# Optimization experiments

Hardware: AMD Instinct MI355X
Metric: run time of the kernel (lower is better)

Reference implementation:

```python
import jax, jax.numpy as jnp
import numpy as np

L, M, DIN, DEM, DH, GH, DOUT = 4, 4, 128, 64, 400, 256, 8
B = 16384
EPS = 1e-5


def setup_inputs() -> dict:
    key = jax.random.key(0)
    ks = iter(jax.random.split(key, 48))
    def p(shape, s=0.05):
        return jax.random.normal(next(ks), shape, jnp.float32) * s
    return dict(
        x=p((B, DIN), 1.0), embedding_input=p((B, DEM), 1.0),
        base_w1=p((DIN, DH)), base_b1=p((DH,)), base_w2=p((DH, DH)), base_b2=p((DH,)),
        em_w=p((DEM, DH)), em_b=p((DH,)),
        gfc_w1=p((DH, GH)), gfc_b1=p((GH,)), gfc_w2=p((GH, GH)), gfc_b2=p((GH,)),
        gw0_w=p((GH, M * M)), gw0_b=p((M * M,)),
        cond1_w=p((M * M, GH)), cond1_b=p((GH,)), gw1_w=p((GH, M * M)), gw1_b=p((M * M,)),
        cond2_w=p((2 * M * M, GH)), cond2_b=p((GH,)), gw2_w=p((GH, M * M)), gw2_b=p((M * M,)),
        condL_w=p((3 * M * M, GH)), condL_b=p((GH,)), gwL_w=p((GH, M)), gwL_b=p((M,)),
        bn1_g=1.0 + p((L, M, DH)), bn1_b=p((L, M, DH)),
        mod_W=p((L, M, DH, DH)), mod_b=p((L, M, DH)),
        bn2_g=1.0 + p((L, M, DH)), bn2_b=p((L, M, DH)),
        last_w=p((DH, DOUT)), last_b=p((DOUT,)),
    )


def _bn(h, g, b):
    # training-mode BatchNorm1d over batch axis; h:[B,M,D], g,b:[M,D]
    mu = h.mean(axis=0)
    var = ((h - mu) ** 2).mean(axis=0)  # biased variance, as torch BN
    return (h - mu) / jnp.sqrt(var + EPS) * g + b


def reference(x, embedding_input,
              base_w1, base_b1, base_w2, base_b2, em_w, em_b,
              gfc_w1, gfc_b1, gfc_w2, gfc_b2,
              gw0_w, gw0_b, cond1_w, cond1_b, gw1_w, gw1_b,
              cond2_w, cond2_b, gw2_w, gw2_b,
              condL_w, condL_b, gwL_w, gwL_b,
              bn1_g, bn1_b, mod_W, mod_b, bn2_g, bn2_b,
              last_w, last_b):
    relu = jax.nn.relu
    b = x.shape[0]
    # base MLP (last activation = identity)
    out = relu(x @ base_w1 + base_b1) @ base_w2 + base_b2          # [B,DH]
    # embedding MLP (single layer, identity last activation)
    emb = embedding_input @ em_w + em_b                            # [B,DH]
    emb = emb * out                                                # cond_ob
    out = relu(out)
    # gating trunk
    emb = relu(emb)
    emb = relu(emb @ gfc_w1 + gfc_b1)
    emb = emb @ gfc_w2 + gfc_b2                                    # [B,GH]
    # routing weight 0
    raw0 = relu(emb) @ gw0_w + gw0_b                               # [B,M*M]
    w0 = jax.nn.softmax(raw0.reshape(b, M, M), axis=-1)
    weights = [w0]
    flat = [w0.reshape(b, M * M)]
    # cascaded routing weights (num_layers-2 = 2 extra)
    for cw, cb, gw, gb in ((cond1_w, cond1_b, gw1_w, gw1_b),
                           (cond2_w, cond2_b, gw2_w, gw2_b)):
        cond = jnp.concatenate(flat, axis=-1) @ cw + cb            # [B,GH]
        cond = relu(cond * emb)
        w = jax.nn.softmax((cond @ gw + gb).reshape(b, M, M), axis=-1)
        weights.append(w)
        flat.append(w.reshape(b, M * M))
    # last (per-module) gating weight
    cond = jnp.concatenate(flat, axis=-1) @ condL_w + condL_b
    cond = relu(cond * emb)
    last_weight = jax.nn.softmax(cond @ gwL_w + gwL_b, axis=-1)    # [B,M]
    # module layer 0: all modules see the same input
    h = jnp.broadcast_to(out[:, None, :], (b, M, DH))
    h = _bn(h, bn1_g[0], bn1_b[0])
    mo = jnp.einsum('bmi,mio->bmo', h, mod_W[0]) + mod_b[0]
    mo = _bn(mo, bn2_g[0], bn2_b[0])                               # [B,M,DH]
    # cascaded module layers with soft routing
    for i in range(1, L):
        mi = relu(jnp.einsum('bkd,bjk->bjd', mo, weights[i - 1]))  # dispatch/combine
        h = _bn(mi, bn1_g[i], bn1_b[i])
        mo = jnp.einsum('bmi,mio->bmo', h, mod_W[i]) + mod_b[i]
        mo = _bn(mo, bn2_g[i], bn2_b[i])
    out = relu(jnp.einsum('bmd,bm->bd', mo, last_weight))
    return out @ last_w + last_b
```

## Files before the change

kernel.cpp:

```cpp
#include <hip/hip_runtime.h>
#include <hip/hip_bf16.h>

typedef __bf16 bf16_t;
typedef __bf16 bf16x8 __attribute__((ext_vector_type(8)));
typedef __bf16 bf16x4 __attribute__((ext_vector_type(4)));
typedef float  f32x4  __attribute__((ext_vector_type(4)));

#define BN_   16384
#define DIN_  128
#define DEM_  64
#define DH_   400
#define DHP_  416
#define DHA_  512
#define GH_   256
#define MM_   4
#define EPS_  1e-5f
#define PCOLS 448
#define NCH   128
#define NCHMI 256

__global__ __launch_bounds__(256) void k_detect_probe(const unsigned* __restrict__ w,
                                                      int* __restrict__ flag,
                                                      int* __restrict__ layC)
{
  __shared__ int cnt[256];
  int c = 0;
  for (int i = 0; i < 16; ++i) {
    unsigned v = w[threadIdx.x * 16 + i];
    float lo = __uint_as_float((v & 0xffffu) << 16);
    if (!(fabsf(lo) < 1e4f)) ++c;
  }
  cnt[threadIdx.x] = c;
  __syncthreads();
  if (threadIdx.x == 0) {
    int t = 0;
    for (int i = 0; i < 256; ++i) t += cnt[i];
    flag[0] = (t > 64) ? 1 : 0;
  }
  if (threadIdx.x < 64) {
    int l = threadIdx.x;
    bf16x8 av, bv;
#pragma unroll
    for (int e = 0; e < 8; ++e) { av[e] = (bf16_t)0.f; bv[e] = (bf16_t)0.f; }
    if ((l >> 4) == 0) av[0] = (bf16_t)(float)(l & 15);
    if (l == 0)        bv[0] = (bf16_t)1.f;
    f32x4 acc = {0.f, 0.f, 0.f, 0.f};
    acc = __builtin_amdgcn_mfma_f32_16x16x32_bf16(av, bv, acc, 0, 0, 0);
    if (l == 1) layC[0] = (acc[0] > 0.5f) ? 1 : 0;
  }
}

#define NS_ 26
struct SmallTab {
  const void* src[NS_];
  bf16_t*     dst[NS_];
  int         n[NS_];
};

struct Cvt2 {
  const void* src1; bf16_t* dst1; int n1;
  const void* src2; bf16_t* dst2; int n2;
};

#define NT_ 9
#define CVZ 8
struct TransTab {
  const void* src[NT_];
  bf16_t*     dst[NT_];
  int K[NT_], N[NT_], KP[NT_], NPa[NT_], usef[NT_];
};

__global__ __launch_bounds__(256) void k_transAll(TransTab tt, SmallTab st, Cvt2 cv,
                                                  const int* __restrict__ flag)
{
  __shared__ float T[64][65];
  const int z = blockIdx.z;
  if (z > NT_) {
    const int f = flag[0];
    const int slice = z - NT_ - 1;
    const int flat = slice * 56 + blockIdx.y * 7 + blockIdx.x;
    const int total = cv.n1 + cv.n2;
    for (int i = flat * 256 + threadIdx.x; i < total; i += 56 * CVZ * 256) {
      if (i < cv.n1)
        cv.dst1[i] = f ? (bf16_t)((const float*)cv.src1)[i] : ((const bf16_t*)cv.src1)[i];
      else {
        int j = i - cv.n1;
        cv.dst2[j] = f ? (bf16_t)((const float*)cv.src2)[j] : ((const bf16_t*)cv.src2)[j];
      }
    }
    return;
  }
  if (z == NT_) {
    const int f = flag[0];
    const int flat = blockIdx.y * 7 + blockIdx.x;
    if (flat >= NS_) return;
    const void* s = st.src[flat];
    bf16_t*     d = st.dst[flat];
    const int   n = st.n[flat];
    for (int i = threadIdx.x; i < n; i += 256)
      d[i] = f ? (bf16_t)((const float*)s)[i] : ((const bf16_t*)s)[i];
    return;
  }
  const int K = tt.K[z], N = tt.N[z], KP = tt.KP[z], NPa = tt.NPa[z];
  const int k0 = blockIdx.x * 64, n0 = blockIdx.y * 64;
  if (k0 >= KP || n0 >= NPa) return;
  const int f = tt.usef[z] ? flag[0] : 0;
  const float*  sf = (const float*) tt.src[z];
  const bf16_t* sb = (const bf16_t*)tt.src[z];
  bf16_t* dp = tt.dst[z];
  const int lr = threadIdx.x >> 6, ln = threadIdx.x & 63;
#pragma unroll
  for (int p = 0; p < 16; ++p) {
    int kl = p * 4 + lr;
    int k = k0 + kl, n = n0 + ln;
    float v = 0.f;
    if (k < K && n < N)
      v = f ? sf[(size_t)k * N + n] : (float)sb[(size_t)k * N + n];
    T[kl][ln] = v;
  }
  __syncthreads();
#pragma unroll
  for (int p = 0; p < 16; ++p) {
    int nl = p * 4 + lr;
    int n = n0 + nl, k = k0 + ln;
    if (n < NPa && k < KP) dp[(size_t)n * KP + k] = (bf16_t)T[ln][nl];
  }
}

__global__ __launch_bounds__(256) void k_prepW(
    const void* __restrict__ modW, size_t off, const bf16_t* __restrict__ modb,
    const float* __restrict__ s1v, const float* __restrict__ t1v,
    bf16_t* __restrict__ WtM, float* __restrict__ bM,
    const int* __restrict__ flag)
{
  __shared__ float T[64][65];
  const int f = flag[0];
  const int m = blockIdx.z;
  if (blockIdx.y == 8) {
    float* ls = &T[0][0];
    const int ncg = blockIdx.x;
    const int t = threadIdx.x;
    const int n = ncg * 64 + (t & 63);
    const int ks = t >> 6;
    float a = 0.f;
    if (n < DH_) {
      for (int k = ks * 100; k < ks * 100 + 100; ++k) {
        size_t idx = off + ((size_t)m * DH_ + k) * DH_ + n;
        float wv = f ? ((const float*)modW)[idx] : (float)((const bf16_t*)modW)[idx];
        a += t1v[m * DHP_ + k] * wv;
      }
    }
    ls[t] = a;
    __syncthreads();
    if (t < 64) {
      int nn = ncg * 64 + t;
      float v = ls[t] + ls[t + 64] + ls[t + 128] + ls[t + 192];
      if (nn < DH_) v += (float)modb[m * DH_ + nn];
      else v = 0.f;
      bM[m * DHA_ + nn] = v;
    }
    if (ncg == 6 && t < 64) bM[m * DHA_ + 448 + t] = 0.f;
    return;
  }
  const float*  sf = (const float*) modW + off + (size_t)m * DH_ * DH_;
  const bf16_t* sb = (const bf16_t*)modW + off + (size_t)m * DH_ * DH_;
  bf16_t* dp = WtM + (size_t)m * DHA_ * DHP_;
  const int k0 = blockIdx.x * 64, n0 = blockIdx.y * 64;
  const int lr = threadIdx.x >> 6, ln = threadIdx.x & 63;
#pragma unroll
  for (int p = 0; p < 16; ++p) {
    int kl = p * 4 + lr;
    int k = k0 + kl, n = n0 + ln;
    float v = 0.f;
    if (k < DH_ && n < DH_)
      v = f ? sf[(size_t)k * DH_ + n] : (float)sb[(size_t)k * DH_ + n];
    if (k < DH_) v *= s1v[m * DHP_ + k];
    T[kl][ln] = v;
  }
  __syncthreads();
#pragma unroll
  for (int p = 0; p < 16; ++p) {
    int nl = p * 4 + lr;
    int n = n0 + nl, k = k0 + ln;
    if (n < DHA_ && k < DHP_) dp[(size_t)n * DHP_ + k] = (bf16_t)T[ln][nl];
  }
}

__device__ __forceinline__ void gload_lds16(const bf16_t* g, bf16_t* l) {
#if __has_builtin(__builtin_amdgcn_global_load_lds)
  __builtin_amdgcn_global_load_lds((const __attribute__((address_space(1))) void*)g,
                                   (__attribute__((address_space(3))) void*)l, 16, 0, 0);
#else
  *(bf16x8*)l = *(const bf16x8*)g;
#endif
}

__device__ __forceinline__ void stage128x32(const bf16_t* __restrict__ g, int ld,
                                            bf16_t* lds, int t) {
  const int c1 = t + 256;
  const int q0 = ((t  & 3) ^ ((t  >> 3) & 3)) * 8;
  const int q1 = ((c1 & 3) ^ ((c1 >> 3) & 3)) * 8;
  gload_lds16(g + (size_t)(t  >> 2) * ld + q0, lds + t  * 8);
  gload_lds16(g + (size_t)(c1 >> 2) * ld + q1, lds + c1 * 8);
}

__device__ __forceinline__ void acc_zero(f32x4 (&acc)[4][4]) {
  const f32x4 z = {0.f, 0.f, 0.f, 0.f};
#pragma unroll
  for (int i = 0; i < 4; ++i)
#pragma unroll
    for (int j = 0; j < 4; ++j) acc[i][j] = z;
}

template<int KS>
__device__ __forceinline__ void gemm_staged(
    const bf16_t* __restrict__ ga, int lda,
    const bf16_t* __restrict__ gb, int ldb,
    bf16_t* ldsA, bf16_t* ldsB,
    int wr, int wc, int rr, int qq, int t,
    f32x4 (&acc)[4][4])
{
  const int qs = (qq ^ ((rr >> 1) & 3)) * 8;
  stage128x32(ga, lda, ldsA, t);
  stage128x32(gb, ldb, ldsB, t);
  int cur = 0;
#pragma unroll 1
  for (int ks = 0; ks < KS; ++ks) {
    __syncthreads();
    if (ks + 1 < KS) {
      stage128x32(ga + (ks + 1) * 32, lda, ldsA + (cur ^ 1) * 4096, t);
      stage128x32(gb + (ks + 1) * 32, ldb, ldsB + (cur ^ 1) * 4096, t);
    }
    const bf16_t* la = ldsA + cur * 4096;
    const bf16_t* lb = ldsB + cur * 4096;
    bf16x8 av[4], bv[4];
#pragma unroll
    for (int i = 0; i < 4; ++i)
      av[i] = *reinterpret_cast<const bf16x8*>(la + (wr + i * 16 + rr) * 32 + qs);
#pragma unroll
    for (int i = 0; i < 4; ++i)
      bv[i] = *reinterpret_cast<const bf16x8*>(lb + (wc + i * 16 + rr) * 32 + qs);
#pragma unroll
    for (int i = 0; i < 4; ++i)
#pragma unroll
      for (int j = 0; j < 4; ++j)
        acc[i][j] = __builtin_amdgcn_mfma_f32_16x16x32_bf16(av[i], bv[j], acc[i][j], 0, 0, 0);
    cur ^= 1;
  }
  __syncthreads();
}

__device__ __forceinline__ void gemm_staged_rt(
    const bf16_t* __restrict__ ga, int lda,
    const bf16_t* __restrict__ gb, int ldb,
    bf16_t* ldsA, bf16_t* ldsB,
    int wr, int wc, int rr, int qq, int t, int KS,
    f32x4 (&acc)[4][4])
{
  const int qs = (qq ^ ((rr >> 1) & 3)) * 8;
  stage128x32(ga, lda, ldsA, t);
  stage128x32(gb, ldb, ldsB, t);
  int cur = 0;
#pragma unroll 1
  for (int ks = 0; ks < KS; ++ks) {
    __syncthreads();
    if (ks + 1 < KS) {
      stage128x32(ga + (ks + 1) * 32, lda, ldsA + (cur ^ 1) * 4096, t);
      stage128x32(gb + (ks + 1) * 32, ldb, ldsB + (cur ^ 1) * 4096, t);
    }
    const bf16_t* la = ldsA + cur * 4096;
    const bf16_t* lb = ldsB + cur * 4096;
    bf16x8 av[4], bv[4];
#pragma unroll
    for (int i = 0; i < 4; ++i)
      av[i] = *reinterpret_cast<const bf16x8*>(la + (wr + i * 16 + rr) * 32 + qs);
#pragma unroll
    for (int i = 0; i < 4; ++i)
      bv[i] = *reinterpret_cast<const bf16x8*>(lb + (wc + i * 16 + rr) * 32 + qs);
#pragma unroll
    for (int i = 0; i < 4; ++i)
#pragma unroll
      for (int j = 0; j < 4; ++j)
        acc[i][j] = __builtin_amdgcn_mfma_f32_16x16x32_bf16(av[i], bv[j], acc[i][j], 0, 0, 0);
    cur ^= 1;
  }
  __syncthreads();
}

template<int KS, bool RELU, bool OUTF32>
__global__ __launch_bounds__(256, 4) void k_gemm_bias(
    const bf16_t* __restrict__ A, int lda,
    const bf16_t* __restrict__ Bt, int ldb,
    const bf16_t* __restrict__ bias, int nbias,
    void* __restrict__ outv, int ldo, int nout,
    const int* __restrict__ layC)
{
  __shared__ bf16_t sAB[4 * 4096];
  const int lay = layC[0];
  const int t = threadIdx.x;
  const int w = t >> 6, lane = t & 63;
  const int rr = lane & 15, qq = lane >> 4;
  const int wr = (w >> 1) * 64, wc = (w & 1) * 64;
  const int rowT = blockIdx.x * 128, colT = blockIdx.y * 128;
  f32x4 acc[4][4]; acc_zero(acc);
  gemm_staged<KS>(A + (size_t)rowT * lda, lda, Bt + (size_t)colT * ldb, ldb,
                  sAB, sAB + 8192, wr, wc, rr, qq, t, acc);
  const int row0 = rowT + wr, col0 = colT + wc;
  float bjv[4];
#pragma unroll
  for (int j = 0; j < 4; ++j) {
    int c = col0 + j * 16 + rr;
    bjv[j] = (c < nbias) ? (float)bias[c] : 0.f;
  }
  if (lay == 0 && !OUTF32) {
    bf16_t* eld = sAB + w * 2304;
#pragma unroll
    for (int p = 0; p < 2; ++p) {
#pragma unroll
      for (int ii = 0; ii < 2; ++ii) {
        int i = p * 2 + ii;
#pragma unroll
        for (int j = 0; j < 4; ++j) {
#pragma unroll
          for (int e = 0; e < 4; ++e) {
            float v = acc[i][j][e] + bjv[j];
            if (RELU) v = fmaxf(v, 0.f);
            eld[(ii * 16 + qq * 4 + e) * 72 + j * 16 + rr] = (bf16_t)v;
          }
        }
      }
#pragma unroll
      for (int rb = 0; rb < 4; ++rb) {
        int rl = rb * 8 + (lane >> 3);
        int c8 = (lane & 7) * 8;
        bf16x8 vv = *reinterpret_cast<const bf16x8*>(eld + rl * 72 + c8);
        int row = row0 + p * 32 + rl;
        int col = colT + wc + c8;
        if (col < nout)
          *reinterpret_cast<bf16x8*>((bf16_t*)outv + (size_t)row * ldo + col) = vv;
      }
    }
  } else {
#pragma unroll
    for (int j = 0; j < 4; ++j) {
#pragma unroll
      for (int i = 0; i < 4; ++i) {
#pragma unroll
        for (int e = 0; e < 4; ++e) {
          int ri = lay ? rr : qq * 4 + e;
          int ci = lay ? qq * 4 + e : rr;
          int row = row0 + i * 16 + ri;
          int col = col0 + j * 16 + ci;
          if (col >= nout) continue;
          float bv = (col < nbias) ? (float)bias[col] : 0.f;
          float v = acc[i][j][e] + bv;
          if (RELU) v = fmaxf(v, 0.f);
          if (OUTF32) ((float*)outv)[(size_t)row * ldo + col] = v;
          else ((bf16_t*)outv)[(size_t)row * ldo + col] = (bf16_t)v;
        }
      }
    }
  }
}

__global__ __launch_bounds__(256, 4) void k_gemm_front_pair(
    const bf16_t* __restrict__ A0, const bf16_t* __restrict__ A1,
    const bf16_t* __restrict__ B0, const bf16_t* __restrict__ B1,
    const bf16_t* __restrict__ bias0, const bf16_t* __restrict__ bias1,
    bf16_t* __restrict__ o0, bf16_t* __restrict__ o1,
    const int* __restrict__ layC)
{
  __shared__ bf16_t sAB[4 * 4096];
  const int z = blockIdx.z;
  const bf16_t* A    = z ? A1 : A0;
  const bf16_t* Bt   = z ? B1 : B0;
  const bf16_t* bias = z ? bias1 : bias0;
  bf16_t* outv       = z ? o1 : o0;
  const int  ld   = z ? DEM_ : DIN_;
  const int  KS   = z ? 2 : 4;
  const bool relu = (z == 0);
  const int lay = layC[0];
  const int t = threadIdx.x;
  const int w = t >> 6, lane = t & 63;
  const int rr = lane & 15, qq = lane >> 4;
  const int wr = (w >> 1) * 64, wc = (w & 1) * 64;
  const int rowT = blockIdx.x * 128, colT = blockIdx.y * 128;
  f32x4 acc[4][4]; acc_zero(acc);
  gemm_staged_rt(A + (size_t)rowT * ld, ld, Bt + (size_t)colT * ld, ld,
                 sAB, sAB + 8192, wr, wc, rr, qq, t, KS, acc);
  const int row0 = rowT + wr, col0 = colT + wc;
  float bjv[4];
#pragma unroll
  for (int j = 0; j < 4; ++j) {
    int c = col0 + j * 16 + rr;
    bjv[j] = (c < DH_) ? (float)bias[c] : 0.f;
  }
  if (lay == 0) {
    bf16_t* eld = sAB + w * 2304;
#pragma unroll
    for (int p = 0; p < 2; ++p) {
#pragma unroll
      for (int ii = 0; ii < 2; ++ii) {
        int i = p * 2 + ii;
#pragma unroll
        for (int j = 0; j < 4; ++j) {
#pragma unroll
          for (int e = 0; e < 4; ++e) {
            float v = acc[i][j][e] + bjv[j];
            if (relu) v = fmaxf(v, 0.f);
            eld[(ii * 16 + qq * 4 + e) * 72 + j * 16 + rr] = (bf16_t)v;
          }
        }
      }
#pragma unroll
      for (int rb = 0; rb < 4; ++rb) {
        int rl = rb * 8 + (lane >> 3);
        int c8 = (lane & 7) * 8;
        bf16x8 vv = *reinterpret_cast<const bf16x8*>(eld + rl * 72 + c8);
        int row = row0 + p * 32 + rl;
        int col = colT + wc + c8;
        if (col < DHP_)
          *reinterpret_cast<bf16x8*>(outv + (size_t)row * DHP_ + col) = vv;
      }
    }
  } else {
#pragma unroll
    for (int j = 0; j < 4; ++j) {
#pragma unroll
      for (int i = 0; i < 4; ++i) {
#pragma unroll
        for (int e = 0; e < 4; ++e) {
          int row = row0 + i * 16 + rr;
          int col = col0 + j * 16 + qq * 4 + e;
          if (col >= DHP_) continue;
          float bv = (col < DH_) ? (float)bias[col] : 0.f;
          float v = acc[i][j][e] + bv;
          if (relu) v = fmaxf(v, 0.f);
          outv[(size_t)row * DHP_ + col] = (bf16_t)v;
        }
      }
    }
  }
}

__global__ __launch_bounds__(256, 4) void k_gemm_base2(
    const bf16_t* __restrict__ A, const bf16_t* __restrict__ Bt,
    const bf16_t* __restrict__ bias, const bf16_t* __restrict__ emb0,
    bf16_t* __restrict__ outA, bf16_t* __restrict__ emb1,
    float* __restrict__ ps, float* __restrict__ pq,
    const int* __restrict__ layC)
{
  __shared__ bf16_t sAB[4 * 4096];
  __shared__ float rs[2][128], rq[2][128];
  const int lay = layC[0];
  const int t = threadIdx.x;
  const int w = t >> 6, lane = t & 63;
  const int rr = lane & 15, qq = lane >> 4;
  const int wr = (w >> 1) * 64, wc = (w & 1) * 64;
  const int rowT = blockIdx.x * 128, colT = blockIdx.y * 128;
  f32x4 acc[4][4]; acc_zero(acc);
  gemm_staged<13>(A + (size_t)rowT * DHP_, DHP_, Bt + (size_t)colT * DHP_, DHP_,
                  sAB, sAB + 8192, wr, wc, rr, qq, t, acc);
  const int row0 = rowT + wr, col0 = colT + wc;
  float bjv[4];
  bool cok[4];
#pragma unroll
  for (int j = 0; j < 4; ++j) {
    int c = col0 + j * 16 + rr;
    bjv[j] = (c < DH_) ? (float)bias[c] : 0.f;
    cok[j] = (c < DHP_);
  }
  float s[4] = {0.f, 0.f, 0.f, 0.f}, q[4] = {0.f, 0.f, 0.f, 0.f};
  if (lay == 0) {
#pragma unroll
    for (int j = 0; j < 4; ++j) {
      if (!cok[j]) continue;
#pragma unroll
      for (int i = 0; i < 4; ++i)
#pragma unroll
        for (int e = 0; e < 4; ++e) {
          float o = fmaxf(acc[i][j][e] + bjv[j], 0.f);
          s[j] += o; q[j] += o * o;
        }
    }
    float* fld = reinterpret_cast<float*>(sAB) + w * 1088;
#pragma unroll
    for (int i = 0; i < 4; ++i) {
#pragma unroll
      for (int j = 0; j < 4; ++j)
#pragma unroll
        for (int e = 0; e < 4; ++e)
          fld[(qq * 4 + e) * 68 + j * 16 + rr] = acc[i][j][e] + bjv[j];
#pragma unroll
      for (int rb = 0; rb < 4; ++rb) {
        int rl = rb * 4 + (lane >> 4);
        int c4 = (lane & 15) * 4;
        f32x4 op4 = *reinterpret_cast<const f32x4*>(fld + rl * 68 + c4);
        int row = row0 + i * 16 + rl;
        int col = colT + wc + c4;
        if (col < DHP_) {
          bf16x4 e04 = *reinterpret_cast<const bf16x4*>(emb0 + (size_t)row * DHP_ + col);
          bf16x4 oA4, e14;
#pragma unroll
          for (int e = 0; e < 4; ++e) {
            float op = op4[e];
            oA4[e] = (bf16_t)fmaxf(op, 0.f);
            e14[e] = (bf16_t)fmaxf((float)e04[e] * op, 0.f);
          }
          *reinterpret_cast<bf16x4*>(outA + (size_t)row * DHP_ + col) = oA4;
          *reinterpret_cast<bf16x4*>(emb1 + (size_t)row * DHP_ + col) = e14;
        }
      }
    }
  } else {
#pragma unroll
    for (int j = 0; j < 4; ++j) {
#pragma unroll
      for (int i = 0; i < 4; ++i) {
#pragma unroll
        for (int e = 0; e < 4; ++e) {
          int ri = rr;
          int ci = qq * 4 + e;
          int row = row0 + i * 16 + ri;
          int col = col0 + j * 16 + ci;
          if (col >= DHP_) continue;
          float bv = (col < DH_) ? (float)bias[col] : 0.f;
          float op = acc[i][j][e] + bv;
          float o  = fmaxf(op, 0.f);
          float e0 = (float)emb0[(size_t)row * DHP_ + col];
          float m1 = fmaxf(e0 * op, 0.f);
          outA[(size_t)row * DHP_ + col] = (bf16_t)o;
          emb1[(size_t)row * DHP_ + col] = (bf16_t)m1;
        }
      }
    }
  }
#pragma unroll
  for (int j = 0; j < 4; ++j) {
    s[j] += __shfl_xor(s[j], 16); s[j] += __shfl_xor(s[j], 32);
    q[j] += __shfl_xor(q[j], 16); q[j] += __shfl_xor(q[j], 32);
  }
  if (lane < 16) {
#pragma unroll
    for (int j = 0; j < 4; ++j) {
      rs[w >> 1][(w & 1) * 64 + j * 16 + lane] = s[j];
      rq[w >> 1][(w & 1) * 64 + j * 16 + lane] = q[j];
    }
  }
  __syncthreads();
  if (lay == 0 && t < 128) {
    int col = blockIdx.y * 128 + t;
    if (col < PCOLS) {
      ps[((size_t)blockIdx.x * MM_ + 0) * PCOLS + col] = rs[0][t] + rs[1][t];
      pq[((size_t)blockIdx.x * MM_ + 0) * PCOLS + col] = rq[0][t] + rq[1][t];
    }
  }
}

__global__ __launch_bounds__(256, 4) void k_gemm_mod(
    const bf16_t* __restrict__ Abase, int lda, int mstride,
    const bf16_t* __restrict__ WtM, const float* __restrict__ bM,
    bf16_t* __restrict__ mo,
    float* __restrict__ ps, float* __restrict__ pq,
    const int* __restrict__ layC)
{
  __shared__ bf16_t sAB[4 * 4096];
  __shared__ float rs[2][128], rq[2][128];
  const int lay = layC[0];
  const int m = blockIdx.z;
  const int t = threadIdx.x;
  const int w = t >> 6, lane = t & 63;
  const int rr = lane & 15, qq = lane >> 4;
  const int wr = (w >> 1) * 64, wc = (w & 1) * 64;
  const int rowT = blockIdx.x * 128, colT = blockIdx.y * 128;
  f32x4 acc[4][4]; acc_zero(acc);
  gemm_staged<13>(Abase + (size_t)m * mstride + (size_t)rowT * lda, lda,
                  WtM + (size_t)m * DHA_ * DHP_ + (size_t)colT * DHP_, DHP_,
                  sAB, sAB + 8192, wr, wc, rr, qq, t, acc);
  const int row0 = rowT + wr, col0 = colT + wc;
  float bjv[4];
  bool cok[4];
#pragma unroll
  for (int j = 0; j < 4; ++j) {
    int c = col0 + j * 16 + rr;
    bjv[j] = bM[m * DHA_ + c];
    cok[j] = (c < DHP_);
  }
  float s[4] = {0.f, 0.f, 0.f, 0.f}, q[4] = {0.f, 0.f, 0.f, 0.f};
  if (lay == 0) {
#pragma unroll
    for (int j = 0; j < 4; ++j) {
      if (!cok[j]) continue;
#pragma unroll
      for (int i = 0; i < 4; ++i)
#pragma unroll
        for (int e = 0; e < 4; ++e) {
          float v = acc[i][j][e] + bjv[j];
          s[j] += v; q[j] += v * v;
        }
    }
    bf16_t* eld = sAB + w * 2304;
#pragma unroll
    for (int p = 0; p < 2; ++p) {
#pragma unroll
      for (int ii = 0; ii < 2; ++ii) {
        int i = p * 2 + ii;
#pragma unroll
        for (int j = 0; j < 4; ++j)
#pragma unroll
          for (int e = 0; e < 4; ++e)
            eld[(ii * 16 + qq * 4 + e) * 72 + j * 16 + rr] = (bf16_t)(acc[i][j][e] + bjv[j]);
      }
#pragma unroll
      for (int rb = 0; rb < 4; ++rb) {
        int rl = rb * 8 + (lane >> 3);
        int c8 = (lane & 7) * 8;
        bf16x8 vv = *reinterpret_cast<const bf16x8*>(eld + rl * 72 + c8);
        int row = row0 + p * 32 + rl;
        int col = colT + wc + c8;
        if (col < DHP_)
          *reinterpret_cast<bf16x8*>(mo + ((size_t)row * MM_ + m) * DHP_ + col) = vv;
      }
    }
  } else {
#pragma unroll
    for (int j = 0; j < 4; ++j) {
#pragma unroll
      for (int i = 0; i < 4; ++i) {
#pragma unroll
        for (int e = 0; e < 4; ++e) {
          int row = row0 + i * 16 + rr;
          int col = col0 + j * 16 + qq * 4 + e;
          if (col >= DHP_) continue;
          float v = acc[i][j][e] + bM[m * DHA_ + col];
          mo[((size_t)row * MM_ + m) * DHP_ + col] = (bf16_t)v;
        }
      }
    }
  }
#pragma unroll
  for (int j = 0; j < 4; ++j) {
    s[j] += __shfl_xor(s[j], 16); s[j] += __shfl_xor(s[j], 32);
    q[j] += __shfl_xor(q[j], 16); q[j] += __shfl_xor(q[j], 32);
  }
  if (lane < 16) {
#pragma unroll
    for (int j = 0; j < 4; ++j) {
      rs[w >> 1][(w & 1) * 64 + j * 16 + lane] = s[j];
      rq[w >> 1][(w & 1) * 64 + j * 16 + lane] = q[j];
    }
  }
  __syncthreads();
  if (lay == 0 && t < 128) {
    int col = blockIdx.y * 128 + t;
    if (col < PCOLS) {
      ps[((size_t)blockIdx.x * MM_ + m) * PCOLS + col] = rs[0][t] + rs[1][t];
      pq[((size_t)blockIdx.x * MM_ + m) * PCOLS + col] = rq[0][t] + rq[1][t];
    }
  }
}

template<int NCHT>
__global__ __launch_bounds__(512) void k_bnprep2(
    const float* __restrict__ ps, const float* __restrict__ pq, int per_m,
    const bf16_t* __restrict__ g, const bf16_t* __restrict__ b,
    float* __restrict__ s_o, float* __restrict__ t_o)
{
  __shared__ float lS[8][64], lQ[8][64];
  const int m = blockIdx.x, cg = blockIdx.y;
  const int sub = threadIdx.x >> 6, lane = threadIdx.x & 63;
  const int k = cg * 64 + lane;
  const int mm = per_m ? m : 0;
  float S = 0.f, Q = 0.f;
#pragma unroll 8
  for (int ch = sub; ch < NCHT; ch += 8) {
    size_t idx = ((size_t)ch * MM_ + mm) * PCOLS + k;
    S += ps[idx];
    Q += pq[idx];
  }
  lS[sub][lane] = S; lQ[sub][lane] = Q;
  __syncthreads();
  if (sub == 0 && k < DHP_) {
    float St = 0.f, Qt = 0.f;
#pragma unroll
    for (int i = 0; i < 8; ++i) { St += lS[i][lane]; Qt += lQ[i][lane]; }
    float s = 0.f, t = 0.f;
    if (k < DH_) {
      float mean = St * (1.f / BN_);
      float var  = fmaxf(Qt * (1.f / BN_) - mean * mean, 0.f);
      float rstd = rsqrtf(var + EPS_);
      s = (float)g[m * DH_ + k] * rstd;
      t = (float)b[m * DH_ + k] - mean * s;
    }
    s_o[m * DHP_ + k] = s;
    t_o[m * DHP_ + k] = t;
  }
}

__global__ __launch_bounds__(256) void k_mix(
    const bf16_t* __restrict__ mo, const float* __restrict__ s2v, const float* __restrict__ t2v,
    const float* __restrict__ wbuf, int woff, bf16_t* __restrict__ mi,
    float* __restrict__ ps, float* __restrict__ pq)
{
  __shared__ float sB[4 * 416], qB[4 * 416];
  const int ch = blockIdx.x;
  const int wave = threadIdx.x >> 6, lane = threadIdx.x & 63;
  const int d0 = lane * 8;
  float sx[4][8], tx[4][8];
  float sAcc[4][8], qAcc[4][8];
#pragma unroll
  for (int j = 0; j < 4; ++j)
#pragma unroll
    for (int e = 0; e < 8; ++e) { sAcc[j][e] = 0.f; qAcc[j][e] = 0.f; }
  if (lane < 52) {
#pragma unroll
    for (int k = 0; k < 4; ++k)
#pragma unroll
      for (int e = 0; e < 8; ++e) {
        sx[k][e] = s2v[k * DHP_ + d0 + e];
        tx[k][e] = t2v[k * DHP_ + d0 + e];
      }
  }
#pragma unroll 1
  for (int i = 0; i < 16; ++i) {
    int b = ch * 64 + wave + i * 4;
    float wv = (lane < 16) ? wbuf[(size_t)b * 52 + woff + lane] : 0.f;
    if (lane < 52) {
      float x[4][8];
#pragma unroll
      for (int k = 0; k < 4; ++k) {
        bf16x8 v = *reinterpret_cast<const bf16x8*>(mo + ((size_t)b * MM_ + k) * DHP_ + d0);
#pragma unroll
        for (int e = 0; e < 8; ++e)
          x[k][e] = (float)v[e] * sx[k][e] + tx[k][e];
      }
#pragma unroll
      for (int j = 0; j < 4; ++j) {
        float w0 = __shfl(wv, j * 4 + 0), w1 = __shfl(wv, j * 4 + 1);
        float w2 = __shfl(wv, j * 4 + 2), w3 = __shfl(wv, j * 4 + 3);
        bf16x8 ov;
#pragma unroll
        for (int e = 0; e < 8; ++e) {
          float a = fmaxf(x[0][e] * w0 + x[1][e] * w1 + x[2][e] * w2 + x[3][e] * w3, 0.f);
          ov[e] = (bf16_t)a;
          float r = (float)ov[e];
          sAcc[j][e] += r; qAcc[j][e] += r * r;
        }
        *reinterpret_cast<bf16x8*>(mi + ((size_t)b * MM_ + j) * DHP_ + d0) = ov;
      }
    }
  }
#pragma unroll 1
  for (int w = 0; w < 4; ++w) {
    if (wave == w && lane < 52) {
#pragma unroll
      for (int j = 0; j < 4; ++j)
#pragma unroll
        for (int e = 0; e < 8; ++e) {
          int idx = j * 416 + d0 + e;
          if (w == 0) { sB[idx] = sAcc[j][e]; qB[idx] = qAcc[j][e]; }
          else        { sB[idx] += sAcc[j][e]; qB[idx] += qAcc[j][e]; }
        }
    }
    __syncthreads();
  }
  for (int idx = threadIdx.x; idx < 4 * 416; idx += 256) {
    int j = idx / 416, col = idx - j * 416;
    ps[((size_t)ch * MM_ + j) * PCOLS + col] = sB[idx];
    pq[((size_t)ch * MM_ + j) * PCOLS + col] = qB[idx];
  }
}

__global__ __launch_bounds__(256) void k_gate(
    const bf16_t* __restrict__ emb,
    const bf16_t* __restrict__ gw0t, const bf16_t* __restrict__ gw0_b,
    const bf16_t* __restrict__ c1_w,  const bf16_t* __restrict__ c1_b,
    const bf16_t* __restrict__ gw1t, const bf16_t* __restrict__ gw1_b,
    const bf16_t* __restrict__ c2_w,  const bf16_t* __restrict__ c2_b,
    const bf16_t* __restrict__ gw2t, const bf16_t* __restrict__ gw2_b,
    const bf16_t* __restrict__ cL_w,  const bf16_t* __restrict__ cL_b,
    const bf16_t* __restrict__ gwLt, const bf16_t* __restrict__ gwL_b,
    float* __restrict__ wbuf)
{
  __shared__ float VBA[4][272], VBB[4][272];
  __shared__ float FLA[4][64], FLB[4][64];
  const int wave = threadIdx.x >> 6, lane = threadIdx.x & 63;
  float* vbA = VBA[wave];
  float* vbB = VBB[wave];
  float* flA = FLA[wave];
  float* flB = FLB[wave];
  const int bA = blockIdx.x * 8 + wave * 2, bB = bA + 1;
  const int wrIdx = lane * 4 + (lane >> 4) * 4;

  float eA[4], eB[4];
  {
    bf16x4 evA = *reinterpret_cast<const bf16x4*>(emb + (size_t)bA * GH_ + lane * 4);
    bf16x4 evB = *reinterpret_cast<const bf16x4*>(emb + (size_t)bB * GH_ + lane * 4);
    f32x4 rA, rB;
#pragma unroll
    for (int e = 0; e < 4; ++e) {
      eA[e] = (float)evA[e]; rA[e] = fmaxf(eA[e], 0.f);
      eB[e] = (float)evB[e]; rB[e] = fmaxf(eB[e], 0.f);
    }
    *reinterpret_cast<f32x4*>(vbA + wrIdx) = rA;
    *reinterpret_cast<f32x4*>(vbB + wrIdx) = rB;
  }
  __builtin_amdgcn_wave_barrier();

  const int hh = lane >> 4, jj = lane & 15;

  auto softmax4 = [&](float a) -> float {
    float m1 = fmaxf(a, __shfl_xor(a, 1));
    float mx = fmaxf(m1, __shfl_xor(m1, 2));
    float ex = __expf(a - mx);
    float sx = ex + __shfl_xor(ex, 1);
    float sm = sx + __shfl_xor(sx, 2);
    return ex / sm;
  };

  auto gw_phase = [&](const bf16_t* Wt, const bf16_t* Bb, int foff) {
    float a0A = 0.f, a1A = 0.f, a0B = 0.f, a1B = 0.f;
#pragma unroll
    for (int cc = 0; cc < 8; ++cc) {
      int c8 = (cc + hh * 2) & 7;
      int k  = hh * 64 + c8 * 8;
      int idx = k + hh * 4;
      f32x4 vA0 = *reinterpret_cast<const f32x4*>(vbA + idx);
      f32x4 vA1 = *reinterpret_cast<const f32x4*>(vbA + idx + 4);
      f32x4 vB0 = *reinterpret_cast<const f32x4*>(vbB + idx);
      f32x4 vB1 = *reinterpret_cast<const f32x4*>(vbB + idx + 4);
      bf16x8 wv = *reinterpret_cast<const bf16x8*>(Wt + jj * 256 + k);
      float w0 = (float)wv[0], w1 = (float)wv[1], w2 = (float)wv[2], w3 = (float)wv[3];
      float w4 = (float)wv[4], w5 = (float)wv[5], w6 = (float)wv[6], w7 = (float)wv[7];
      a0A = fmaf(vA0[0], w0, a0A); a0A = fmaf(vA0[1], w1, a0A);
      a0A = fmaf(vA0[2], w2, a0A); a0A = fmaf(vA0[3], w3, a0A);
      a1A = fmaf(vA1[0], w4, a1A); a1A = fmaf(vA1[1], w5, a1A);
      a1A = fmaf(vA1[2], w6, a1A); a1A = fmaf(vA1[3], w7, a1A);
      a0B = fmaf(vB0[0], w0, a0B); a0B = fmaf(vB0[1], w1, a0B);
      a0B = fmaf(vB0[2], w2, a0B); a0B = fmaf(vB0[3], w3, a0B);
      a1B = fmaf(vB1[0], w4, a1B); a1B = fmaf(vB1[1], w5, a1B);
      a1B = fmaf(vB1[2], w6, a1B); a1B = fmaf(vB1[3], w7, a1B);
    }
    float aA = a0A + a1A, aB = a0B + a1B;
    aA += __shfl_xor(aA, 16); aA += __shfl_xor(aA, 32);
    aB += __shfl_xor(aB, 16); aB += __shfl_xor(aB, 32);
    float bb = (float)Bb[jj];
    aA += bb; aB += bb;
    float wA = softmax4(aA), wB = softmax4(aB);
    if (lane < 16) {
      flA[foff + jj] = wA; wbuf[(size_t)bA * 52 + foff + jj] = wA;
      flB[foff + jj] = wB; wbuf[(size_t)bB * 52 + foff + jj] = wB;
    }
    __builtin_amdgcn_wave_barrier();
  };

  auto cond_phase = [&](const bf16_t* W, const bf16_t* Bb, int tcount) {
    float a4A[4], a4B[4];
    bf16x4 bb = *reinterpret_cast<const bf16x4*>(Bb + lane * 4);
#pragma unroll
    for (int e = 0; e < 4; ++e) { a4A[e] = (float)bb[e]; a4B[e] = a4A[e]; }
    for (int t = 0; t < tcount; ++t) {
      float fA = flA[t], fB = flB[t];
      bf16x4 wv = *reinterpret_cast<const bf16x4*>(W + t * 256 + lane * 4);
#pragma unroll
      for (int e = 0; e < 4; ++e) {
        float w = (float)wv[e];
        a4A[e] = fmaf(fA, w, a4A[e]);
        a4B[e] = fmaf(fB, w, a4B[e]);
      }
    }
    f32x4 rA, rB;
#pragma unroll
    for (int e = 0; e < 4; ++e) {
      rA[e] = fmaxf(a4A[e] * eA[e], 0.f);
      rB[e] = fmaxf(a4B[e] * eB[e], 0.f);
    }
    *reinterpret_cast<f32x4*>(vbA + wrIdx) = rA;
    *reinterpret_cast<f32x4*>(vbB + wrIdx) = rB;
    __builtin_amdgcn_wave_barrier();
  };

  gw_phase(gw0t, gw0_b, 0);
  cond_phase(c1_w, c1_b, 16);
  gw_phase(gw1t, gw1_b, 16);
  cond_phase(c2_w, c2_b, 32);
  gw_phase(gw2t, gw2_b, 32);
  cond_phase(cL_w, cL_b, 48);
  {
    const int j4 = lane & 3, h16 = lane >> 2;
    const int base = h16 * 16 + (h16 >> 2) * 4;
    bf16x8 w0 = *reinterpret_cast<const bf16x8*>(gwLt + j4 * 256 + h16 * 16);
    bf16x8 w1 = *reinterpret_cast<const bf16x8*>(gwLt + j4 * 256 + h16 * 16 + 8);
    float aA = 0.f, aB = 0.f;
#pragma unroll
    for (int c = 0; c < 2; ++c) {
      f32x4 vA0 = *reinterpret_cast<const f32x4*>(vbA + base + c * 8);
      f32x4 vA1 = *reinterpret_cast<const f32x4*>(vbA + base + c * 8 + 4);
      f32x4 vB0 = *reinterpret_cast<const f32x4*>(vbB + base + c * 8);
      f32x4 vB1 = *reinterpret_cast<const f32x4*>(vbB + base + c * 8 + 4);
      const bf16x8& w = c ? w1 : w0;
#pragma unroll
      for (int e = 0; e < 4; ++e) {
        aA = fmaf(vA0[e], (float)w[e], aA);
        aA = fmaf(vA1[e], (float)w[e + 4], aA);
        aB = fmaf(vB0[e], (float)w[e], aB);
        aB = fmaf(vB1[e], (float)w[e + 4], aB);
      }
    }
    aA += __shfl_xor(aA, 4); aA += __shfl_xor(aA, 8);
    aA += __shfl_xor(aA, 16); aA += __shfl_xor(aA, 32);
    aB += __shfl_xor(aB, 4); aB += __shfl_xor(aB, 8);
    aB += __shfl_xor(aB, 16); aB += __shfl_xor(aB, 32);
    float bb = (float)gwL_b[j4];
    aA += bb; aB += bb;
    float wA = softmax4(aA), wB = softmax4(aB);
    if (lane < 4) {
      wbuf[(size_t)bA * 52 + 48 + j4] = wA;
      wbuf[(size_t)bB * 52 + 48 + j4] = wB;
    }
  }
}

__global__ __launch_bounds__(256) void k_final(
    const bf16_t* __restrict__ mo, const float* __restrict__ s2v, const float* __restrict__ t2v,
    const float* __restrict__ wbuf, const bf16_t* __restrict__ last_w,
    const bf16_t* __restrict__ last_b, void* __restrict__ outv,
    const int* __restrict__ flag)
{
  const int f32out = flag[0];
  const int wave = threadIdx.x >> 6, lane = threadIdx.x & 63;
  const int d0 = lane * 8;
  float sx[4][8], tx[4][8];
  if (lane < 52) {
#pragma unroll
    for (int k = 0; k < 4; ++k)
#pragma unroll
      for (int e = 0; e < 8; ++e) {
        sx[k][e] = s2v[k * DHP_ + d0 + e];
        tx[k][e] = t2v[k * DHP_ + d0 + e];
      }
  }
  for (int b = blockIdx.x * 4 + wave; b < BN_; b += gridDim.x * 4) {
    const float* lwp = wbuf + (size_t)b * 52 + 48;
    float lm0 = lwp[0], lm1 = lwp[1], lm2 = lwp[2], lm3 = lwp[3];
    float slm = lm0 + lm1 + lm2 + lm3;
    const float* w0p = wbuf + (size_t)b * 52;
    float sw0 = w0p[0] + w0p[1] + w0p[2] + w0p[3];
    float p[8];
#pragma unroll
    for (int j = 0; j < 8; ++j) p[j] = 0.f;
    if (lane < 52) {
      float x[4][8];
#pragma unroll
      for (int k = 0; k < 4; ++k) {
        bf16x8 v = *reinterpret_cast<const bf16x8*>(mo + ((size_t)b * MM_ + k) * DHP_ + d0);
#pragma unroll
        for (int e = 0; e < 8; ++e)
          x[k][e] = (float)v[e] * sx[k][e] + tx[k][e];
      }
#pragma unroll
      for (int e = 0; e < 8; ++e) {
        float v = fmaxf(x[0][e] * lm0 + x[1][e] * lm1 + x[2][e] * lm2 + x[3][e] * lm3, 0.f);
        bf16x8 wv = *reinterpret_cast<const bf16x8*>(last_w + (size_t)(d0 + e) * 8);
#pragma unroll
        for (int j = 0; j < 8; ++j) p[j] = fmaf(v, (float)wv[j], p[j]);
      }
    }
#pragma unroll
    for (int j = 0; j < 8; ++j) {
      p[j] += __shfl_xor(p[j], 1);
      p[j] += __shfl_xor(p[j], 2);
      p[j] += __shfl_xor(p[j], 4);
      p[j] += __shfl_xor(p[j], 8);
      p[j] += __shfl_xor(p[j], 16);
      p[j] += __shfl_xor(p[j], 32);
    }
    float sel = p[0];
#pragma unroll
    for (int j = 1; j < 8; ++j) if (lane == j) sel = p[j];
    if (lane < 8) {
      float res = sel + (float)last_b[lane];
      if (!(fabsf(res) < 1e4f)) res = 400.f;
      if (!(slm > 0.97f && slm < 1.03f)) res = 1000.f;
      if (!(sw0 > 0.97f && sw0 < 1.03f)) res = 2000.f;
      if (f32out) ((float*)outv)[(size_t)b * 8 + lane] = res;
      else ((bf16_t*)outv)[(size_t)b * 8 + lane] = (bf16_t)res;
    }
  }
}

extern "C" void kernel_launch(void* const* d_in, const int* in_sizes, int n_in,
                              void* d_out, int out_size, void* d_ws, size_t ws_size,
                              hipStream_t stream)
{
  (void)in_sizes; (void)n_in;
  const void* x_raw   = d_in[0];
  const void* emb_raw = d_in[1];
  const void* base_w1 = d_in[2];
  const void* base_w2 = d_in[4];
  const void* em_w    = d_in[6];
  const void* gfc_w1  = d_in[8];
  const void* gfc_w2  = d_in[10];
  const void* modW_raw= d_in[28];

  char* base = (char*)d_ws;
  size_t off = 0;
  auto alloc = [&](size_t bytes) -> char* {
    off = (off + 255) & ~(size_t)255;
    char* r = base + off; off += bytes; return r;
  };
  int*    dflag = (int*)   alloc(16);
  int*    layC  = (int*)   alloc(16);
  bf16_t* Wt1  = (bf16_t*)alloc((size_t)512 * 128 * 2);
  bf16_t* Wem  = (bf16_t*)alloc((size_t)512 * 64 * 2);
  bf16_t* Wt2  = (bf16_t*)alloc((size_t)512 * DHP_ * 2);
  bf16_t* Wg1  = (bf16_t*)alloc((size_t)256 * DHP_ * 2);
  bf16_t* Wg2  = (bf16_t*)alloc((size_t)256 * 256 * 2);
  bf16_t* WtM  = (bf16_t*)alloc((size_t)MM_ * DHA_ * DHP_ * 2);
  float*  bM   = (float*) alloc((size_t)MM_ * DHA_ * 4);
  bf16_t* xc   = (bf16_t*)alloc((size_t)BN_ * DIN_ * 2);
  bf16_t* embc = (bf16_t*)alloc((size_t)BN_ * DEM_ * 2);
  bf16_t* out1 = (bf16_t*)alloc((size_t)BN_ * DHP_ * 2);
  bf16_t* emb0 = (bf16_t*)alloc((size_t)BN_ * DHP_ * 2);
  bf16_t* outA = (bf16_t*)alloc((size_t)BN_ * DHP_ * 2);
  bf16_t* emb1 = (bf16_t*)alloc((size_t)BN_ * DHP_ * 2);
  bf16_t* embF = (bf16_t*)alloc((size_t)BN_ * GH_ * 2);
  float*  wbuf = (float*) alloc((size_t)BN_ * 52 * 4);
  bf16_t* mo   = (bf16_t*)alloc((size_t)BN_ * MM_ * DHP_ * 2);
  bf16_t* mi   = (bf16_t*)alloc((size_t)BN_ * MM_ * DHP_ * 2);
  float* psO = (float*)alloc((size_t)NCH * MM_ * PCOLS * 4);
  float* pqO = (float*)alloc((size_t)NCH * MM_ * PCOLS * 4);
  float* psA = (float*)alloc((size_t)NCHMI * MM_ * PCOLS * 4);
  float* pqA = (float*)alloc((size_t)NCHMI * MM_ * PCOLS * 4);
  float* psB = (float*)alloc((size_t)NCH * MM_ * PCOLS * 4);
  float* pqB = (float*)alloc((size_t)NCH * MM_ * PCOLS * 4);
  float* s1 = (float*)alloc((size_t)MM_ * DHP_ * 4);
  float* t1 = (float*)alloc((size_t)MM_ * DHP_ * 4);
  float* s2 = (float*)alloc((size_t)MM_ * DHP_ * 4);
  float* t2 = (float*)alloc((size_t)MM_ * DHP_ * 4);
  bf16_t* gw0t = (bf16_t*)alloc((size_t)16 * 256 * 2);
  bf16_t* gw1t = (bf16_t*)alloc((size_t)16 * 256 * 2);
  bf16_t* gw2t = (bf16_t*)alloc((size_t)16 * 256 * 2);
  bf16_t* gwLt = (bf16_t*)alloc((size_t)4 * 256 * 2);
  const int sn[NS_] = {400, 400, 400, 256, 256,
                       4096, 16, 4096, 256, 4096, 16, 8192, 256, 4096, 16,
                       12288, 256, 1024, 4,
                       6400, 6400, 6400, 6400, 6400, 3200, 8};
  const int si[NS_] = {3, 5, 7, 9, 11,
                       12, 13, 14, 15, 16, 17, 18, 19, 20, 21,
                       22, 23, 24, 25,
                       26, 27, 29, 30, 31, 32, 33};
  bf16_t* sc[NS_];
  for (int i = 0; i < NS_; ++i) sc[i] = (bf16_t*)alloc((size_t)sn[i] * 2);
  bf16_t *b1c = sc[0], *b2c = sc[1], *embbc = sc[2], *g1bc = sc[3], *g2bc = sc[4];
  bf16_t *gw0b = sc[6], *c1w = sc[7], *c1b = sc[8],
         *gw1b = sc[10], *c2w = sc[11], *c2b = sc[12], *gw2b = sc[14],
         *cLw = sc[15], *cLb = sc[16], *gwLb = sc[18];
  bf16_t *bn1g = sc[19], *bn1b = sc[20], *modbc = sc[21], *bn2g = sc[22], *bn2b = sc[23];
  bf16_t *lastw = sc[24], *lastb = sc[25];

  if (off > ws_size) {
    hipMemsetAsync(d_out, 0, (size_t)out_size * 2, stream);
    return;
  }

  dim3 blk(256);
  k_detect_probe<<<1, blk, 0, stream>>>((const unsigned*)x_raw, dflag, layC);

  SmallTab tab;
  for (int i = 0; i < NS_; ++i) { tab.src[i] = d_in[si[i]]; tab.dst[i] = sc[i]; tab.n[i] = sn[i]; }
  Cvt2 cv;
  cv.src1 = x_raw;   cv.dst1 = xc;   cv.n1 = BN_ * DIN_;
  cv.src2 = emb_raw; cv.dst2 = embc; cv.n2 = BN_ * DEM_;
  TransTab tt;
  tt.src[0] = base_w1;  tt.dst[0] = Wt1;  tt.K[0] = DIN_; tt.N[0] = DH_; tt.KP[0] = 128;  tt.NPa[0] = 512; tt.usef[0] = 1;
  tt.src[1] = em_w;     tt.dst[1] = Wem;  tt.K[1] = DEM_; tt.N[1] = DH_; tt.KP[1] = 64;   tt.NPa[1] = 512; tt.usef[1] = 1;
  tt.src[2] = base_w2;  tt.dst[2] = Wt2;  tt.K[2] = DH_;  tt.N[2] = DH_; tt.KP[2] = DHP_; tt.NPa[2] = 512; tt.usef[2] = 1;
  tt.src[3] = gfc_w1;   tt.dst[3] = Wg1;  tt.K[3] = DH_;  tt.N[3] = GH_; tt.KP[3] = DHP_; tt.NPa[3] = 256; tt.usef[3] = 1;
  tt.src[4] = gfc_w2;   tt.dst[4] = Wg2;  tt.K[4] = GH_;  tt.N[4] = GH_; tt.KP[4] = 256;  tt.NPa[4] = 256; tt.usef[4] = 1;
  tt.src[5] = d_in[12]; tt.dst[5] = gw0t; tt.K[5] = 256;  tt.N[5] = 16;  tt.KP[5] = 256;  tt.NPa[5] = 16;  tt.usef[5] = 1;
  tt.src[6] = d_in[16]; tt.dst[6] = gw1t; tt.K[6] = 256;  tt.N[6] = 16;  tt.KP[6] = 256;  tt.NPa[6] = 16;  tt.usef[6] = 1;
  tt.src[7] = d_in[20]; tt.dst[7] = gw2t; tt.K[7] = 256;  tt.N[7] = 16;  tt.KP[7] = 256;  tt.NPa[7] = 16;  tt.usef[7] = 1;
  tt.src[8] = d_in[24]; tt.dst[8] = gwLt; tt.K[8] = 256;  tt.N[8] = 4;   tt.KP[8] = 256;  tt.NPa[8] = 4;   tt.usef[8] = 1;
  k_transAll<<<dim3(7, 8, NT_ + 1 + CVZ), blk, 0, stream>>>(tt, tab, cv, dflag);

  k_gemm_front_pair<<<dim3(128, 4, 2), blk, 0, stream>>>(
      xc, embc, Wt1, Wem, b1c, embbc, out1, emb0, layC);
  k_gemm_base2<<<dim3(128, 4), blk, 0, stream>>>(out1, Wt2, b2c, emb0, outA, emb1, psO, pqO, layC);
  bf16_t* emb2 = emb0;
  k_gemm_bias<13, true , false><<<dim3(128, 2), blk, 0, stream>>>(emb1, DHP_, Wg1, DHP_, g1bc, GH_, emb2, GH_, GH_, layC);
  k_gemm_bias<8,  false, false><<<dim3(128, 2), blk, 0, stream>>>(emb2, GH_, Wg2, GH_, g2bc, GH_, embF, GH_, GH_, layC);

  k_gate<<<dim3(BN_ / 8), blk, 0, stream>>>(embF,
      gw0t, gw0b, c1w, c1b, gw1t, gw1b, c2w, c2b, gw2t, gw2b,
      cLw, cLb, gwLt, gwLb, wbuf);

  k_bnprep2<NCH><<<dim3(4, 7), dim3(512), 0, stream>>>(psO, pqO, 0, bn1g, bn1b, s1, t1);
  k_prepW<<<dim3(7, 9, 4), blk, 0, stream>>>(modW_raw, 0, modbc, s1, t1, WtM, bM, dflag);
  k_gemm_mod<<<dim3(128, 4, 4), blk, 0, stream>>>(outA, DHP_, 0, WtM, bM, mo, psB, pqB, layC);

  for (int L = 1; L < 4; ++L) {
    k_bnprep2<NCH><<<dim3(4, 7), dim3(512), 0, stream>>>(psB, pqB, 1,
        bn2g + (size_t)(L - 1) * MM_ * DH_, bn2b + (size_t)(L - 1) * MM_ * DH_, s2, t2);
    k_mix<<<dim3(NCHMI), blk, 0, stream>>>(mo, s2, t2, wbuf, (L - 1) * 16, mi, psA, pqA);
    k_bnprep2<NCHMI><<<dim3(4, 7), dim3(512), 0, stream>>>(psA, pqA, 1,
        bn1g + (size_t)L * MM_ * DH_, bn1b + (size_t)L * MM_ * DH_, s1, t1);
    k_prepW<<<dim3(7, 9, 4), blk, 0, stream>>>(modW_raw, (size_t)L * MM_ * DH_ * DH_,
                                               modbc + (size_t)L * MM_ * DH_, s1, t1, WtM, bM, dflag);
    k_gemm_mod<<<dim3(128, 4, 4), blk, 0, stream>>>(mi, MM_ * DHP_, DHP_, WtM, bM, mo, psB, pqB, layC);
  }

  k_bnprep2<NCH><<<dim3(4, 7), dim3(512), 0, stream>>>(psB, pqB, 1,
      bn2g + (size_t)3 * MM_ * DH_, bn2b + (size_t)3 * MM_ * DH_, s2, t2);
  k_final<<<dim3(1024), blk, 0, stream>>>(mo, s2, t2, wbuf, lastw, lastb, d_out, dflag);
}
```

Baseline: 511.4 us.

## Fuse BatchNorm stat reduction into producer kernels via last-blocks atomic counter

Removes the separate k_bnprep2 launches by having each stats-producing kernel (base2, gemm_mod, mix) bump a global atomic ticket at the end. The last 28 blocks to arrive spin until all blocks have finished, then reduce the partial sums and write the BN scale and shift. This removes about 9 small kernel launches and their gaps. In exchange it adds a spin-wait in those tail blocks and relies on a per-forward memset of the counters. The ps/pq writes are guarded by lay==0 while the fold runs unconditionally, which is consistent only if lay is 0 in practice.

```diff
diff --git a/kernel.cpp b/kernel.cpp
--- a/kernel.cpp
+++ b/kernel.cpp
@@ -124,6 +124,57 @@
     int nl = p * 4 + lr;
     int n = n0 + nl, k = k0 + ln;
     if (n < NPa && k < KP) dp[(size_t)n * KP + k] = (bf16_t)T[ln][nl];
+  }
+}
+
+__device__ __forceinline__ void bn_fold_tail(
+    unsigned* ctr, unsigned target, int tid, float* scratch, unsigned* sTickP,
+    const float* __restrict__ ps, const float* __restrict__ pq, int nch, int per_m,
+    const bf16_t* __restrict__ g, const bf16_t* __restrict__ b,
+    float* __restrict__ s_o, float* __restrict__ t_o)
+{
+  __syncthreads();
+  if (tid == 0) {
+    __threadfence();
+    *sTickP = __hip_atomic_fetch_add(ctr, 1u, __ATOMIC_ACQ_REL, __HIP_MEMORY_SCOPE_AGENT);
+  }
+  __syncthreads();
+  unsigned tick = *sTickP;
+  if (tick < target - 28u || tick >= target) return;
+  if (tid == 0) {
+    while (__hip_atomic_load(ctr, __ATOMIC_ACQUIRE, __HIP_MEMORY_SCOPE_AGENT) < target)
+      __builtin_amdgcn_s_sleep(8);
+  }
+  __syncthreads();
+  const int r = (int)(tick - (target - 28u));
+  const int m = r & 3, cg = r >> 2;
+  const int sub = tid >> 6, lane = tid & 63;
+  const int k = cg * 64 + lane;
+  const int mm = per_m ? m : 0;
+  float S = 0.f, Q = 0.f;
+  for (int ch = sub; ch < nch; ch += 4) {
+    size_t idx = ((size_t)ch * MM_ + mm) * PCOLS + k;
+    S += ps[idx]; Q += pq[idx];
+  }
+  scratch[sub * 64 + lane] = S;
+  scratch[256 + sub * 64 + lane] = Q;
+  __syncthreads();
+  if (tid < 64) {
+    int kk = cg * 64 + tid;
+    if (kk < DHP_) {
+      float St = scratch[tid] + scratch[64 + tid] + scratch[128 + tid] + scratch[192 + tid];
+      float Qt = scratch[256 + tid] + scratch[320 + tid] + scratch[384 + tid] + scratch[448 + tid];
+      float s = 0.f, t = 0.f;
+      if (kk < DH_) {
+        float mean = St * (1.f / BN_);
+        float var  = fmaxf(Qt * (1.f / BN_) - mean * mean, 0.f);
+        float rstd = rsqrtf(var + EPS_);
+        s = (float)g[m * DH_ + kk] * rstd;
+        t = (float)b[m * DH_ + kk] - mean * s;
+      }
+      s_o[m * DHP_ + kk] = s;
+      t_o[m * DHP_ + kk] = t;
+    }
   }
 }
 
@@ -448,10 +499,14 @@
     const bf16_t* __restrict__ bias, const bf16_t* __restrict__ emb0,
     bf16_t* __restrict__ outA, bf16_t* __restrict__ emb1,
     float* __restrict__ ps, float* __restrict__ pq,
-    const int* __restrict__ layC)
+    const int* __restrict__ layC,
+    unsigned* __restrict__ ctr,
+    const bf16_t* __restrict__ bng, const bf16_t* __restrict__ bnb,
+    float* __restrict__ s_o, float* __restrict__ t_o)
 {
   __shared__ bf16_t sAB[4 * 4096];
   __shared__ float rs[2][128], rq[2][128];
+  __shared__ unsigned sTick;
   const int lay = layC[0];
   const int t = threadIdx.x;
   const int w = t >> 6, lane = t & 63;
@@ -555,6 +610,8 @@
       pq[((size_t)blockIdx.x * MM_ + 0) * PCOLS + col] = rq[0][t] + rq[1][t];
     }
   }
+  bn_fold_tail(ctr, 128u * 4u, t, reinterpret_cast<float*>(sAB), &sTick,
+               ps, pq, NCH, 0, bng, bnb, s_o, t_o);
 }
 
 __global__ __launch_bounds__(256, 4) void k_gemm_mod(
@@ -562,10 +619,14 @@
     const bf16_t* __restrict__ WtM, const float* __restrict__ bM,
     bf16_t* __restrict__ mo,
     float* __restrict__ ps, float* __restrict__ pq,
-    const int* __restrict__ layC)
+    const int* __restrict__ layC,
+    unsigned* __restrict__ ctr,
+    const bf16_t* __restrict__ bng, const bf16_t* __restrict__ bnb,
+    float* __restrict__ s_o, float* __restrict__ t_o)
 {
   __shared__ bf16_t sAB[4 * 4096];
   __shared__ float rs[2][128], rq[2][128];
+  __shared__ unsigned sTick;
   const int lay = layC[0];
   const int m = blockIdx.z;
   const int t = threadIdx.x;
@@ -658,51 +719,20 @@
       pq[((size_t)blockIdx.x * MM_ + m) * PCOLS + col] = rq[0][t] + rq[1][t];
     }
   }
-}
-
-template<int NCHT>
-__global__ __launch_bounds__(512) void k_bnprep2(
-    const float* __restrict__ ps, const float* __restrict__ pq, int per_m,
-    const bf16_t* __restrict__ g, const bf16_t* __restrict__ b,
-    float* __restrict__ s_o, float* __restrict__ t_o)
-{
-  __shared__ float lS[8][64], lQ[8][64];
-  const int m = blockIdx.x, cg = blockIdx.y;
-  const int sub = threadIdx.x >> 6, lane = threadIdx.x & 63;
-  const int k = cg * 64 + lane;
-  const int mm = per_m ? m : 0;
-  float S = 0.f, Q = 0.f;
-#pragma unroll 8
-  for (int ch = sub; ch < NCHT; ch += 8) {
-    size_t idx = ((size_t)ch * MM_ + mm) * PCOLS + k;
-    S += ps[idx];
-    Q += pq[idx];
-  }
-  lS[sub][lane] = S; lQ[sub][lane] = Q;
-  __syncthreads();
-  if (sub == 0 && k < DHP_) {
-    float St = 0.f, Qt = 0.f;
-#pragma unroll
-    for (int i = 0; i < 8; ++i) { St += lS[i][lane]; Qt += lQ[i][lane]; }
-    float s = 0.f, t = 0.f;
-    if (k < DH_) {
-      float mean = St * (1.f / BN_);
-      float var  = fmaxf(Qt * (1.f / BN_) - mean * mean, 0.f);
-      float rstd = rsqrtf(var + EPS_);
-      s = (float)g[m * DH_ + k] * rstd;
-      t = (float)b[m * DH_ + k] - mean * s;
-    }
-    s_o[m * DHP_ + k] = s;
-    t_o[m * DHP_ + k] = t;
-  }
+  bn_fold_tail(ctr, 128u * 4u * 4u, t, reinterpret_cast<float*>(sAB), &sTick,
+               ps, pq, NCH, 1, bng, bnb, s_o, t_o);
 }
 
 __global__ __launch_bounds__(256) void k_mix(
     const bf16_t* __restrict__ mo, const float* __restrict__ s2v, const float* __restrict__ t2v,
     const float* __restrict__ wbuf, int woff, bf16_t* __restrict__ mi,
-    float* __restrict__ ps, float* __restrict__ pq)
+    float* __restrict__ ps, float* __restrict__ pq,
+    unsigned* __restrict__ ctr,
+    const bf16_t* __restrict__ bng, const bf16_t* __restrict__ bnb,
+    float* __restrict__ s_o, float* __restrict__ t_o)
 {
   __shared__ float sB[4 * 416], qB[4 * 416];
+  __shared__ unsigned sTick;
   const int ch = blockIdx.x;
   const int wave = threadIdx.x >> 6, lane = threadIdx.x & 63;
   const int d0 = lane * 8;
@@ -769,6 +799,8 @@
     ps[((size_t)ch * MM_ + j) * PCOLS + col] = sB[idx];
     pq[((size_t)ch * MM_ + j) * PCOLS + col] = qB[idx];
   }
+  bn_fold_tail(ctr, (unsigned)NCHMI, threadIdx.x, sB, &sTick,
+               ps, pq, NCHMI, 1, bng, bnb, s_o, t_o);
 }
 
 __global__ __launch_bounds__(256) void k_gate(
@@ -1011,6 +1043,7 @@
   };
   int*    dflag = (int*)   alloc(16);
   int*    layC  = (int*)   alloc(16);
+  unsigned* ctrs = (unsigned*)alloc(64);
   bf16_t* Wt1  = (bf16_t*)alloc((size_t)512 * 128 * 2);
   bf16_t* Wem  = (bf16_t*)alloc((size_t)512 * 64 * 2);
   bf16_t* Wt2  = (bf16_t*)alloc((size_t)512 * DHP_ * 2);
@@ -1065,6 +1098,7 @@
   }
 
   dim3 blk(256);
+  hipMemsetAsync(ctrs, 0, 64, stream);
   k_detect_probe<<<1, blk, 0, stream>>>((const unsigned*)x_raw, dflag, layC);
 
   SmallTab tab;
@@ -1086,7 +1120,9 @@
 
   k_gemm_front_pair<<<dim3(128, 4, 2), blk, 0, stream>>>(
       xc, embc, Wt1, Wem, b1c, embbc, out1, emb0, layC);
-  k_gemm_base2<<<dim3(128, 4), blk, 0, stream>>>(out1, Wt2, b2c, emb0, outA, emb1, psO, pqO, layC);
+  k_gemm_base2<<<dim3(128, 4), blk, 0, stream>>>(out1, Wt2, b2c, emb0, outA, emb1,
+                                                 psO, pqO, layC,
+                                                 ctrs + 0, bn1g, bn1b, s1, t1);
   bf16_t* emb2 = emb0;
   k_gemm_bias<13, true , false><<<dim3(128, 2), blk, 0, stream>>>(emb1, DHP_, Wg1, DHP_, g1bc, GH_, emb2, GH_, GH_, layC);
   k_gemm_bias<8,  false, false><<<dim3(128, 2), blk, 0, stream>>>(emb2, GH_, Wg2, GH_, g2bc, GH_, embF, GH_, GH_, layC);
@@ -1095,22 +1131,22 @@
       gw0t, gw0b, c1w, c1b, gw1t, gw1b, c2w, c2b, gw2t, gw2b,
       cLw, cLb, gwLt, gwLb, wbuf);
 
-  k_bnprep2<NCH><<<dim3(4, 7), dim3(512), 0, stream>>>(psO, pqO, 0, bn1g, bn1b, s1, t1);
   k_prepW<<<dim3(7, 9, 4), blk, 0, stream>>>(modW_raw, 0, modbc, s1, t1, WtM, bM, dflag);
-  k_gemm_mod<<<dim3(128, 4, 4), blk, 0, stream>>>(outA, DHP_, 0, WtM, bM, mo, psB, pqB, layC);
+  k_gemm_mod<<<dim3(128, 4, 4), blk, 0, stream>>>(outA, DHP_, 0, WtM, bM, mo, psB, pqB, layC,
+                                                  ctrs + 4, bn2g, bn2b, s2, t2);
 
   for (int L = 1; L < 4; ++L) {
-    k_bnprep2<NCH><<<dim3(4, 7), dim3(512), 0, stream>>>(psB, pqB, 1,
-        bn2g + (size_t)(L - 1) * MM_ * DH_, bn2b + (size_t)(L - 1) * MM_ * DH_, s2, t2);
-    k_mix<<<dim3(NCHMI), blk, 0, stream>>>(mo, s2, t2, wbuf, (L - 1) * 16, mi, psA, pqA);
-    k_bnprep2<NCHMI><<<dim3(4, 7), dim3(512), 0, stream>>>(psA, pqA, 1,
-        bn1g + (size_t)L * MM_ * DH_, bn1b + (size_t)L * MM_ * DH_, s1, t1);
+    k_mix<<<dim3(NCHMI), blk, 0, stream>>>(mo, s2, t2, wbuf, (L - 1) * 16, mi, psA, pqA,
+                                           ctrs + L,
+                                           bn1g + (size_t)L * MM_ * DH_, bn1b + (size_t)L * MM_ * DH_,
+                                           s1, t1);
     k_prepW<<<dim3(7, 9, 4), blk, 0, stream>>>(modW_raw, (size_t)L * MM_ * DH_ * DH_,
                                                modbc + (size_t)L * MM_ * DH_, s1, t1, WtM, bM, dflag);
-    k_gemm_mod<<<dim3(128, 4, 4), blk, 0, stream>>>(mi, MM_ * DHP_, DHP_, WtM, bM, mo, psB, pqB, layC);
-  }
-
-  k_bnprep2<NCH><<<dim3(4, 7), dim3(512), 0, stream>>>(psB, pqB, 1,
-      bn2g + (size_t)3 * MM_ * DH_, bn2b + (size_t)3 * MM_ * DH_, s2, t2);
+    k_gemm_mod<<<dim3(128, 4, 4), blk, 0, stream>>>(mi, MM_ * DHP_, DHP_, WtM, bM, mo, psB, pqB, layC,
+                                                    ctrs + 4 + L,
+                                                    bn2g + (size_t)L * MM_ * DH_, bn2b + (size_t)L * MM_ * DH_,
+                                                    s2, t2);
+  }
+
   k_final<<<dim3(1024), blk, 0, stream>>>(mo, s2, t2, wbuf, lastw, lastb, d_out, dflag);
 }
```

Result: slower. 1.202 ms (+135.1%).
